# Performance work log

Measured on AMD Instinct MI355X. Metric: run time of the kernel, lower is better.

The kernel has to match this reference:

```python
import jax, jax.numpy as jnp
import numpy as np

B, M, D = 8, 8192, 1024   # batch, tokens, latent_dim
N, P = 128, 1             # num_experts, slots_per_expert
F = 4096                  # expert_dim


def setup_inputs() -> dict:
    key = jax.random.key(0)
    k_x, k_phi, k_w1, k_b1, k_w2, k_b2 = jax.random.split(key, 6)
    x = jax.random.normal(k_x, (B, M, D), dtype=jnp.float32)
    # phi initialized as randn(d, n, p) / sqrt(d) in the original
    phi = jax.random.normal(k_phi, (D, N, P), dtype=jnp.float32) / (D ** 0.5)
    # Single shared expert MLP (original aliases one nn.Sequential across all experts)
    W1 = jax.random.normal(k_w1, (D, F), dtype=jnp.float32) / (D ** 0.5)
    b1 = jax.random.normal(k_b1, (F,), dtype=jnp.float32) * 0.01
    W2 = jax.random.normal(k_w2, (F, D), dtype=jnp.float32) / (F ** 0.5)
    b2 = jax.random.normal(k_b2, (D,), dtype=jnp.float32) * 0.01
    return {"x": x, "phi": phi, "W1": W1, "b1": b1, "W2": W2, "b2": b2}


def reference(x, phi, W1, b1, W2, b2):
    # dispatch / combine logits: [b, m, n, p]
    logits = jnp.einsum('bmd,dnp->bmnp', x, phi)
    d = jax.nn.softmax(logits, axis=1)                      # softmax over tokens m
    b_, m_, n_, p_ = logits.shape
    c = jax.nn.softmax(logits.reshape(b_, m_, n_ * p_), axis=-1).reshape(b_, m_, n_, p_)
    # slot inputs: [b, n, p, d]
    x_i = jnp.einsum('bmd,bmnp->bnpd', x, d)
    # shared expert MLP (torch GELU default = exact erf)
    h = jax.nn.gelu(jnp.einsum('bnpd,df->bnpf', x_i, W1) + b1, approximate=False)
    y_i = jnp.einsum('bnpf,fd->bnpd', h, W2) + b2
    # combine: [b, m, d]
    y = jnp.einsum('bnpd,bmnp->bmd', y_i, c)
    return y
```

## Files before the change

### kernel.cpp

```cpp
#include <hip/hip_runtime.h>
#include <math.h>

#define Bq 8
#define Mq 8192
#define Dq 1024
#define Nq 128
#define Fq 4096

typedef __bf16 bf16x8 __attribute__((ext_vector_type(8)));
typedef float f32x4 __attribute__((ext_vector_type(4)));
union P4 { __bf16 h[4]; unsigned long long u; };
union H4 { short4 v; _Float16 h[4]; };
union B8 { int4 v; __bf16 h[8]; };

__device__ __forceinline__ int swz128(int row, int bcol) {
  return row * 128 + (bcol ^ ((row & 7) << 4));
}
__device__ __forceinline__ int swz256(int row, int bcol) {
  return row * 256 + (bcol ^ ((row & 7) << 4));
}
__device__ __forceinline__ int swzX(int row, int bcol) {
  return row * 128 + (bcol ^ ((((row & 7) ^ ((row >> 3) & 7))) << 4));
}

__global__ __launch_bounds__(256) void wconv(const float* __restrict__ src,
                                             unsigned long long* __restrict__ dst, long n4)
{
  long i = (long)blockIdx.x * 256 + threadIdx.x;
  if (i >= n4) return;
  float4 v = ((const float4*)src)[i];
  P4 p; p.h[0] = (__bf16)v.x; p.h[1] = (__bf16)v.y; p.h[2] = (__bf16)v.z; p.h[3] = (__bf16)v.w;
  dst[i] = p.u;
}

__global__ __launch_bounds__(256) void phi_conv(const float* __restrict__ src,
                                                __bf16* __restrict__ dst)
{
  int idx = blockIdx.x * 256 + threadIdx.x;
  int d = idx >> 7, n = idx & 127;
  dst[(long)n * Dq + d] = (__bf16)src[idx];
}

__global__ __launch_bounds__(256) void logits_mfma(
    const float* __restrict__ x, const __bf16* __restrict__ phiT,
    __bf16* __restrict__ eT, __bf16* __restrict__ cbuf)
{
  __shared__ __align__(16) char sA[16384];
  __shared__ __align__(16) char sP[16384];
  int mt = blockIdx.x, b = blockIdx.y;
  int m0 = mt * 128;
  int t = threadIdx.x;
  int arow = t >> 4, ac4 = t & 15;
  int prow = t >> 1, pc = (t & 1) * 4;
  int w = t >> 6, l = t & 63, la = l & 15, lb = l >> 4;

  f32x4 zero = {0.f, 0.f, 0.f, 0.f};
  f32x4 acc[2][8];
  for (int i = 0; i < 2; ++i) for (int j = 0; j < 8; ++j) acc[i][j] = zero;

  for (int k0 = 0; k0 < Dq; k0 += 64) {
    #pragma unroll
    for (int i = 0; i < 8; ++i) {
      int row = arow + 16 * i;
      float4 v = *(const float4*)(x + ((long)b * Mq + m0 + row) * Dq + k0 + ac4 * 4);
      P4 p;
      p.h[0] = (__bf16)v.x; p.h[1] = (__bf16)v.y;
      p.h[2] = (__bf16)v.z; p.h[3] = (__bf16)v.w;
      *(unsigned long long*)(sA + swz128(row, 8 * ac4)) = p.u;
    }
    {
      const __bf16* Pp = phiT + (long)prow * Dq + k0 + pc * 8;
      #pragma unroll
      for (int q = 0; q < 4; ++q)
        *(int4*)(sP + swz128(prow, (pc + q) * 16)) = *(const int4*)(Pp + q * 8);
    }
    __syncthreads();
    #pragma unroll
    for (int sub = 0; sub < 2; ++sub) {
      int mbyte = sub * 64 + lb * 16;
      bf16x8 af0 = *(const bf16x8*)(sA + swz128(w * 32 + la, mbyte));
      bf16x8 af1 = *(const bf16x8*)(sA + swz128(w * 32 + 16 + la, mbyte));
      bf16x8 bv[8];
      #pragma unroll
      for (int j = 0; j < 8; ++j)
        bv[j] = *(const bf16x8*)(sP + swz128(j * 16 + la, mbyte));
      #pragma unroll
      for (int j = 0; j < 8; ++j) {
        acc[0][j] = __builtin_amdgcn_mfma_f32_16x16x32_bf16(af0, bv[j], acc[0][j], 0, 0, 0);
        acc[1][j] = __builtin_amdgcn_mfma_f32_16x16x32_bf16(af1, bv[j], acc[1][j], 0, 0, 0);
      }
    }
    __syncthreads();
  }
  float inv[2][4];
  #pragma unroll
  for (int i = 0; i < 2; ++i)
    #pragma unroll
    for (int r = 0; r < 4; ++r) {
      float s = 0.f;
      #pragma unroll
      for (int j = 0; j < 8; ++j) s += __expf(acc[i][j][r]);
      s += __shfl_xor(s, 1); s += __shfl_xor(s, 2);
      s += __shfl_xor(s, 4); s += __shfl_xor(s, 8);
      inv[i][r] = 1.0f / s;
    }
  __bf16* Cb = cbuf + ((long)b * Mq + m0) * Nq;
  __bf16* Eb = eT + (long)b * Nq * Mq + m0;
  #pragma unroll
  for (int i = 0; i < 2; ++i)
    #pragma unroll
    for (int j = 0; j < 8; ++j) {
      P4 p;
      #pragma unroll
      for (int r = 0; r < 4; ++r) {
        int row = w * 32 + i * 16 + lb * 4 + r;
        float e = __expf(acc[i][j][r]);
        p.h[r] = (__bf16)e;
        Cb[(long)row * Nq + j * 16 + la] = (__bf16)(e * inv[i][r]);
      }
      *(unsigned long long*)(Eb + (long)(j * 16 + la) * Mq + w * 32 + i * 16 + lb * 4) = p.u;
    }
}

__global__ __launch_bounds__(256) void colsum_rows(const __bf16* __restrict__ eT,
                                                   float* __restrict__ cinv)
{
  __shared__ float red[4];
  int r = blockIdx.x;
  int t = threadIdx.x;
  const __bf16* p = eT + (long)r * Mq;
  float s = 0.f;
  #pragma unroll
  for (int k = 0; k < 4; ++k) {
    B8 v; v.v = *(const int4*)(p + t * 8 + k * 2048);
    #pragma unroll
    for (int e = 0; e < 8; ++e) s += (float)v.h[e];
  }
  #pragma unroll
  for (int off = 32; off >= 1; off >>= 1) s += __shfl_down(s, off);
  if ((t & 63) == 0) red[t >> 6] = s;
  __syncthreads();
  if (t == 0) cinv[r] = 1.0f / (red[0] + red[1] + red[2] + red[3]);
}

__global__ __launch_bounds__(256) void xi_mfma(
    const __bf16* __restrict__ eT, const float* __restrict__ x,
    _Float16* __restrict__ part)
{
  __shared__ __align__(16) char sD[16384];
  __shared__ __align__(16) char sX[16384];
  int lin = blockIdx.x;
  int wk = (lin & 7) * 64 + (lin >> 3);
  int dts = wk & 7, kc = (wk >> 3) & 7, b = wk >> 6;
  int d0 = dts * 128;
  int t = threadIdx.x;
  int w = t >> 6, l = t & 63, la = l & 15, lb = l >> 4;
  int arow = t >> 1, ahalf = t & 1;
  const __bf16* Ep0 = eT + ((long)b * Nq + arow) * Mq + kc * 1024 + ahalf * 32;
  int bmb = (w * 2 + (l >> 5)) * 8;
  int bd  = (l & 31) * 4;
  const float* Xp0 = x + ((long)b * Mq + kc * 1024 + bmb) * Dq + d0 + bd;

  f32x4 zero = {0.f, 0.f, 0.f, 0.f};
  f32x4 acc[2][8];
  for (int i = 0; i < 2; ++i) for (int j = 0; j < 8; ++j) acc[i][j] = zero;

  int4 ar[4];
  float br[8][4];
  #pragma unroll
  for (int q = 0; q < 4; ++q) ar[q] = *(const int4*)(Ep0 + q * 8);
  #pragma unroll
  for (int k = 0; k < 8; ++k) *(float4*)br[k] = *(const float4*)(Xp0 + (long)k * Dq);
  #pragma unroll
  for (int q = 0; q < 4; ++q) *(int4*)(sD + swzX(arow, ahalf * 64 + q * 16)) = ar[q];
  #pragma unroll
  for (int q = 0; q < 4; ++q) {
    B8 o;
    #pragma unroll
    for (int k = 0; k < 8; ++k) o.h[k] = (__bf16)br[k][q];
    *(int4*)(sX + swzX(bd + q, 2 * bmb)) = o.v;
  }

  for (int it = 0; it < 16; ++it) {
    __syncthreads();
    if (it < 15) {
      #pragma unroll
      for (int q = 0; q < 4; ++q) ar[q] = *(const int4*)(Ep0 + (it + 1) * 64 + q * 8);
      #pragma unroll
      for (int k = 0; k < 8; ++k)
        *(float4*)br[k] = *(const float4*)(Xp0 + ((long)(it + 1) * 64 + k) * Dq);
    }
    #pragma unroll
    for (int sub = 0; sub < 2; ++sub) {
      int mbyte = sub * 64 + lb * 16;
      bf16x8 af0 = *(const bf16x8*)(sD + swzX(w * 32 + la, mbyte));
      bf16x8 af1 = *(const bf16x8*)(sD + swzX(w * 32 + 16 + la, mbyte));
      #pragma unroll
      for (int j = 0; j < 8; ++j) {
        bf16x8 bv = *(const bf16x8*)(sX + swzX(j * 16 + la, mbyte));
        acc[0][j] = __builtin_amdgcn_mfma_f32_16x16x32_bf16(af0, bv, acc[0][j], 0, 0, 0);
        acc[1][j] = __builtin_amdgcn_mfma_f32_16x16x32_bf16(af1, bv, acc[1][j], 0, 0, 0);
      }
    }
    __syncthreads();
    if (it < 15) {
      #pragma unroll
      for (int q = 0; q < 4; ++q) *(int4*)(sD + swzX(arow, ahalf * 64 + q * 16)) = ar[q];
      #pragma unroll
      for (int q = 0; q < 4; ++q) {
        B8 o;
        #pragma unroll
        for (int k = 0; k < 8; ++k) o.h[k] = (__bf16)br[k][q];
        *(int4*)(sX + swzX(bd + q, 2 * bmb)) = o.v;
      }
    }
  }
  _Float16* P = part + (((long)kc * Bq + b) * 8 + dts) * 16384;
  #pragma unroll
  for (int i = 0; i < 2; ++i)
    #pragma unroll
    for (int j = 0; j < 8; ++j) {
      H4 o;
      #pragma unroll
      for (int r = 0; r < 4; ++r) o.h[r] = (_Float16)acc[i][j][r];
      *(short4*)(P + ((w * 16 + i * 8 + j) * 64 + l) * 4) = o.v;
    }
}

__global__ __launch_bounds__(256) void xi_reduce(const _Float16* __restrict__ part,
    const float* __restrict__ cinv, __bf16* __restrict__ xib)
{
  int s = blockIdx.x * 256 + threadIdx.x;
  int l = s & 63, j = (s >> 6) & 7, i = (s >> 9) & 1;
  int w = (s >> 10) & 3, dts = (s >> 12) & 7, b = s >> 15;
  const _Float16* p = part + ((long)b * 8 + dts) * 16384 + ((w * 16 + i * 8 + j) * 64 + l) * 4;
  float sum[4] = {};
  #pragma unroll
  for (int kc = 0; kc < 8; ++kc) {
    H4 v; v.v = *(const short4*)(p + (long)kc * 1048576);
    #pragma unroll
    for (int r = 0; r < 4; ++r) sum[r] += (float)v.h[r];
  }
  int lb = l >> 4, la = l & 15;
  int nbase = w * 32 + i * 16 + lb * 4;
  int d = dts * 128 + j * 16 + la;
  #pragma unroll
  for (int r = 0; r < 4; ++r) {
    int n = b * 128 + nbase + r;
    xib[(long)n * Dq + d] = (__bf16)(sum[r] * cinv[n]);
  }
}

template<int EPI, typename OT>
__global__ __launch_bounds__(256) void gemm_bf16(const __bf16* __restrict__ A,
    const __bf16* __restrict__ Bw, const float* __restrict__ bias,
    OT* __restrict__ C, int lda, int ldb, int ldc, int kLen, long strideCz)
{
  __shared__ __align__(16) char sA[16384];
  __shared__ __align__(16) char sB[16384];
  int m0 = blockIdx.x * 128, n0 = blockIdx.y * 128;
  int kbase = blockIdx.z * kLen;
  C += (long)blockIdx.z * strideCz;
  int t = threadIdx.x;
  int col = t & 127, half = t >> 7;
  int w = t >> 6, l = t & 63, la = l & 15, lb = l >> 4;

  f32x4 zero = {0.f, 0.f, 0.f, 0.f};
  f32x4 acc[2][8];
  for (int i = 0; i < 2; ++i) for (int j = 0; j < 8; ++j) acc[i][j] = zero;

  for (int kt = 0; kt < kLen; kt += 64) {
    int kp = kbase + kt;
    #pragma unroll
    for (int s = 0; s < 4; ++s) {
      int idx = t + 256 * s;
      int row = idx >> 3, c8 = idx & 7;
      *(int4*)(sA + swz128(row, c8 * 16)) =
          *(const int4*)(A + (long)(m0 + row) * lda + kp + c8 * 8);
    }
    {
      const __bf16* Bp = Bw + (long)(kp + half * 32) * ldb + n0 + col;
      #pragma unroll
      for (int i = 0; i < 32; i += 4) {
        P4 p;
        p.h[0] = Bp[(long)(i + 0) * ldb]; p.h[1] = Bp[(long)(i + 1) * ldb];
        p.h[2] = Bp[(long)(i + 2) * ldb]; p.h[3] = Bp[(long)(i + 3) * ldb];
        *(unsigned long long*)(sB + swz128(col, 2 * (half * 32 + i))) = p.u;
      }
    }
    __syncthreads();
    #pragma unroll
    for (int sub = 0; sub < 2; ++sub) {
      int mbyte = sub * 64 + lb * 16;
      bf16x8 af0 = *(const bf16x8*)(sA + swz128(w * 32 + la, mbyte));
      bf16x8 af1 = *(const bf16x8*)(sA + swz128(w * 32 + 16 + la, mbyte));
      bf16x8 bv[8];
      #pragma unroll
      for (int j = 0; j < 8; ++j)
        bv[j] = *(const bf16x8*)(sB + swz128(j * 16 + la, mbyte));
      #pragma unroll
      for (int j = 0; j < 8; ++j) {
        acc[0][j] = __builtin_amdgcn_mfma_f32_16x16x32_bf16(af0, bv[j], acc[0][j], 0, 0, 0);
        acc[1][j] = __builtin_amdgcn_mfma_f32_16x16x32_bf16(af1, bv[j], acc[1][j], 0, 0, 0);
      }
    }
    __syncthreads();
  }
  #pragma unroll
  for (int i = 0; i < 2; ++i)
    #pragma unroll
    for (int j = 0; j < 8; ++j)
      #pragma unroll
      for (int r = 0; r < 4; ++r) {
        int row = m0 + w * 32 + i * 16 + lb * 4 + r;
        int colg = n0 + j * 16 + la;
        float v = acc[i][j][r];
        if (EPI == 2) {
          v += bias[colg];
          v = 0.5f * v * (1.0f + erff(v * 0.70710678118654752f));
        }
        C[(long)row * ldc + colg] = (OT)v;
      }
}

__global__ __launch_bounds__(256) void g2_reduce(const float* __restrict__ part,
    const float* __restrict__ b2, __bf16* __restrict__ yiT)
{
  long idx = (long)blockIdx.x * 256 + threadIdx.x;
  int row = (int)(idx >> 10);
  int d = (int)(idx & 1023);
  float s = part[idx] + part[idx + 1048576] + part[idx + 2097152] + part[idx + 3145728] + b2[d];
  int b = row >> 7, n = row & 127;
  yiT[((long)b * Dq + d) * Nq + n] = (__bf16)s;
}

__global__ __launch_bounds__(256) void combine_mfma(const __bf16* __restrict__ cbuf,
    const __bf16* __restrict__ yiT, float* __restrict__ y)
{
  __shared__ __align__(16) char sC[32768];
  __shared__ __align__(16) char sY[32768];
  int lin = blockIdx.x;
  int wk = (lin & 7) * 512 + (lin >> 3);
  int dt = wk & 7, mt = (wk >> 3) & 63, b = wk >> 9;
  int m0 = mt * 128, d0 = dt * 128;
  int t = threadIdx.x;
  #pragma unroll
  for (int s = 0; s < 8; ++s) {
    int idx = t + 256 * s;
    int row = idx >> 4, c16 = idx & 15;
    *(int4*)(sC + swz256(row, c16 * 16)) =
        *(const int4*)(cbuf + ((long)b * Mq + m0 + row) * Nq + c16 * 8);
    *(int4*)(sY + swz256(row, c16 * 16)) =
        *(const int4*)(yiT + ((long)b * Dq + d0 + row) * Nq + c16 * 8);
  }
  __syncthreads();
  int w = t >> 6, l = t & 63, la = l & 15, lb = l >> 4;
  f32x4 zero = {0.f, 0.f, 0.f, 0.f};
  f32x4 acc[2][8];
  for (int i = 0; i < 2; ++i) for (int j = 0; j < 8; ++j) acc[i][j] = zero;
  #pragma unroll
  for (int sub = 0; sub < 4; ++sub) {
    int mbyte = sub * 64 + lb * 16;
    bf16x8 af0 = *(const bf16x8*)(sC + swz256(w * 32 + la, mbyte));
    bf16x8 af1 = *(const bf16x8*)(sC + swz256(w * 32 + 16 + la, mbyte));
    #pragma unroll
    for (int j = 0; j < 8; ++j) {
      bf16x8 bv = *(const bf16x8*)(sY + swz256(j * 16 + la, mbyte));
      acc[0][j] = __builtin_amdgcn_mfma_f32_16x16x32_bf16(af0, bv, acc[0][j], 0, 0, 0);
      acc[1][j] = __builtin_amdgcn_mfma_f32_16x16x32_bf16(af1, bv, acc[1][j], 0, 0, 0);
    }
  }
  float* Y = y + ((long)b * Mq + m0) * Dq + d0;
  #pragma unroll
  for (int i = 0; i < 2; ++i)
    #pragma unroll
    for (int j = 0; j < 8; ++j)
      #pragma unroll
      for (int r = 0; r < 4; ++r)
        Y[(long)(w * 32 + i * 16 + lb * 4 + r) * Dq + j * 16 + la] = acc[i][j][r];
}

extern "C" void kernel_launch(void* const* d_in, const int* in_sizes, int n_in,
                              void* d_out, int out_size, void* d_ws, size_t ws_size,
                              hipStream_t stream) {
  const float* x   = (const float*)d_in[0];
  const float* phi = (const float*)d_in[1];
  const float* W1  = (const float*)d_in[2];
  const float* b1  = (const float*)d_in[3];
  const float* W2  = (const float*)d_in[4];
  const float* b2  = (const float*)d_in[5];
  float* y = (float*)d_out;

  char* W = (char*)d_ws;
  __bf16*   cbuf   = (__bf16*)W;
  __bf16*   eT     = (__bf16*)(W + 16777216);
  __bf16*   h      = eT;
  _Float16* part   = (_Float16*)(W + 33554432);
  float*    g2part = (float*)(W + 33554432);
  __bf16*   W1b    = (__bf16*)(W + 50331648);
  __bf16*   W2b    = (__bf16*)(W + 58720256);
  __bf16*   xib    = (__bf16*)(W + 67108864);
  __bf16*   yiT    = (__bf16*)(W + 69206016);
  float*    cinv   = (float*)(W + 71303168);
  __bf16*   phiT   = (__bf16*)(W + 75497472);

  wconv<<<4096, 256, 0, stream>>>(W1, (unsigned long long*)W1b, 1048576);
  wconv<<<4096, 256, 0, stream>>>(W2, (unsigned long long*)W2b, 1048576);
  phi_conv<<<512, 256, 0, stream>>>(phi, phiT);
  logits_mfma<<<dim3(Mq / 128, Bq), 256, 0, stream>>>(x, phiT, eT, cbuf);
  colsum_rows<<<Bq * Nq, 256, 0, stream>>>(eT, cinv);
  xi_mfma<<<512, 256, 0, stream>>>(eT, x, part);
  xi_reduce<<<1024, 256, 0, stream>>>(part, cinv, xib);
  gemm_bf16<2, __bf16><<<dim3(8, 32, 1), 256, 0, stream>>>(
      xib, W1b, b1, h, Dq, Fq, Fq, 1024, 0L);
  gemm_bf16<0, float><<<dim3(8, 8, 4), 256, 0, stream>>>(
      h, W2b, nullptr, g2part, Fq, Dq, Dq, 1024, 1048576L);
  g2_reduce<<<4096, 256, 0, stream>>>(g2part, b2, yiT);
  combine_mfma<<<4096, 256, 0, stream>>>(cbuf, yiT, y);
}
```

Baseline: 365.1 us.

## Pre-transpose weights to bf16 and cache bf16 x copy for xi GEMM

```diff
diff --git a/kernel.cpp b/kernel.cpp
--- a/kernel.cpp
+++ b/kernel.cpp
@@ -12,6 +12,7 @@
 union P4 { __bf16 h[4]; unsigned long long u; };
 union H4 { short4 v; _Float16 h[4]; };
 union B8 { int4 v; __bf16 h[8]; };
+union U4 { ushort4 v; __bf16 h[4]; };
 
 __device__ __forceinline__ int swz128(int row, int bcol) {
   return row * 128 + (bcol ^ ((row & 7) << 4));
@@ -21,16 +22,6 @@
 }
 __device__ __forceinline__ int swzX(int row, int bcol) {
   return row * 128 + (bcol ^ ((((row & 7) ^ ((row >> 3) & 7))) << 4));
-}
-
-__global__ __launch_bounds__(256) void wconv(const float* __restrict__ src,
-                                             unsigned long long* __restrict__ dst, long n4)
-{
-  long i = (long)blockIdx.x * 256 + threadIdx.x;
-  if (i >= n4) return;
-  float4 v = ((const float4*)src)[i];
-  P4 p; p.h[0] = (__bf16)v.x; p.h[1] = (__bf16)v.y; p.h[2] = (__bf16)v.z; p.h[3] = (__bf16)v.w;
-  dst[i] = p.u;
 }
 
 __global__ __launch_bounds__(256) void phi_conv(const float* __restrict__ src,
@@ -41,9 +32,35 @@
   dst[(long)n * Dq + d] = (__bf16)src[idx];
 }
 
+__global__ __launch_bounds__(256) void wconvT(const float* __restrict__ src,
+                                              __bf16* __restrict__ dst, int R, int C)
+{
+  __shared__ __bf16 tile[64][66];
+  int c0 = blockIdx.x * 64, r0 = blockIdx.y * 64;
+  int t = threadIdx.x;
+  int row = t >> 2, cq = (t & 3) * 16;
+  const float* S = src + (long)(r0 + row) * C + c0 + cq;
+  #pragma unroll
+  for (int q = 0; q < 4; ++q) {
+    float4 v = *(const float4*)(S + q * 4);
+    tile[cq + q * 4 + 0][row] = (__bf16)v.x;
+    tile[cq + q * 4 + 1][row] = (__bf16)v.y;
+    tile[cq + q * 4 + 2][row] = (__bf16)v.z;
+    tile[cq + q * 4 + 3][row] = (__bf16)v.w;
+  }
+  __syncthreads();
+  __bf16* D = dst + (long)(c0 + row) * R + r0 + cq;
+  B8 o0, o1;
+  #pragma unroll
+  for (int e = 0; e < 8; ++e) { o0.h[e] = tile[row][cq + e]; o1.h[e] = tile[row][cq + 8 + e]; }
+  *(int4*)(D) = o0.v;
+  *(int4*)(D + 8) = o1.v;
+}
+
+template<bool WXB>
 __global__ __launch_bounds__(256) void logits_mfma(
     const float* __restrict__ x, const __bf16* __restrict__ phiT,
-    __bf16* __restrict__ eT, __bf16* __restrict__ cbuf)
+    __bf16* __restrict__ eT, __bf16* __restrict__ cbuf, __bf16* __restrict__ xb)
 {
   __shared__ __align__(16) char sA[16384];
   __shared__ __align__(16) char sP[16384];
@@ -67,6 +84,8 @@
       p.h[0] = (__bf16)v.x; p.h[1] = (__bf16)v.y;
       p.h[2] = (__bf16)v.z; p.h[3] = (__bf16)v.w;
       *(unsigned long long*)(sA + swz128(row, 8 * ac4)) = p.u;
+      if (WXB)
+        *(unsigned long long*)(xb + ((long)b * Mq + m0 + row) * Dq + k0 + ac4 * 4) = p.u;
     }
     {
       const __bf16* Pp = phiT + (long)prow * Dq + k0 + pc * 8;
@@ -143,8 +162,8 @@
   if (t == 0) cinv[r] = 1.0f / (red[0] + red[1] + red[2] + red[3]);
 }
 
-__global__ __launch_bounds__(256) void xi_mfma(
-    const __bf16* __restrict__ eT, const float* __restrict__ x,
+__global__ __launch_bounds__(256) void xi_mfma_xb(
+    const __bf16* __restrict__ eT, const __bf16* __restrict__ xb,
     _Float16* __restrict__ part)
 {
   __shared__ __align__(16) char sD[16384];
@@ -159,28 +178,111 @@
   const __bf16* Ep0 = eT + ((long)b * Nq + arow) * Mq + kc * 1024 + ahalf * 32;
   int bmb = (w * 2 + (l >> 5)) * 8;
   int bd  = (l & 31) * 4;
-  const float* Xp0 = x + ((long)b * Mq + kc * 1024 + bmb) * Dq + d0 + bd;
+  const __bf16* Xp0 = xb + ((long)b * Mq + kc * 1024 + bmb) * Dq + d0 + bd;
 
   f32x4 zero = {0.f, 0.f, 0.f, 0.f};
   f32x4 acc[2][8];
   for (int i = 0; i < 2; ++i) for (int j = 0; j < 8; ++j) acc[i][j] = zero;
 
   int4 ar[4];
-  float br[8][4];
+  U4 br[8];
   #pragma unroll
   for (int q = 0; q < 4; ++q) ar[q] = *(const int4*)(Ep0 + q * 8);
   #pragma unroll
-  for (int k = 0; k < 8; ++k) *(float4*)br[k] = *(const float4*)(Xp0 + (long)k * Dq);
+  for (int k = 0; k < 8; ++k) br[k].v = *(const ushort4*)(Xp0 + (long)k * Dq);
   #pragma unroll
   for (int q = 0; q < 4; ++q) *(int4*)(sD + swzX(arow, ahalf * 64 + q * 16)) = ar[q];
   #pragma unroll
   for (int q = 0; q < 4; ++q) {
     B8 o;
     #pragma unroll
+    for (int k = 0; k < 8; ++k) o.h[k] = br[k].h[q];
+    *(int4*)(sX + swzX(bd + q, 2 * bmb)) = o.v;
+  }
+
+  for (int it = 0; it < 16; ++it) {
+    __syncthreads();
+    if (it < 15) {
+      #pragma unroll
+      for (int q = 0; q < 4; ++q) ar[q] = *(const int4*)(Ep0 + (it + 1) * 64 + q * 8);
+      #pragma unroll
+      for (int k = 0; k < 8; ++k)
+        br[k].v = *(const ushort4*)(Xp0 + ((long)(it + 1) * 64 + k) * Dq);
+    }
+    #pragma unroll
+    for (int sub = 0; sub < 2; ++sub) {
+      int mbyte = sub * 64 + lb * 16;
+      bf16x8 af0 = *(const bf16x8*)(sD + swzX(w * 32 + la, mbyte));
+      bf16x8 af1 = *(const bf16x8*)(sD + swzX(w * 32 + 16 + la, mbyte));
+      #pragma unroll
+      for (int j = 0; j < 8; ++j) {
+        bf16x8 bv = *(const bf16x8*)(sX + swzX(j * 16 + la, mbyte));
+        acc[0][j] = __builtin_amdgcn_mfma_f32_16x16x32_bf16(af0, bv, acc[0][j], 0, 0, 0);
+        acc[1][j] = __builtin_amdgcn_mfma_f32_16x16x32_bf16(af1, bv, acc[1][j], 0, 0, 0);
+      }
+    }
+    __syncthreads();
+    if (it < 15) {
+      #pragma unroll
+      for (int q = 0; q < 4; ++q) *(int4*)(sD + swzX(arow, ahalf * 64 + q * 16)) = ar[q];
+      #pragma unroll
+      for (int q = 0; q < 4; ++q) {
+        B8 o;
+        #pragma unroll
+        for (int k = 0; k < 8; ++k) o.h[k] = br[k].h[q];
+        *(int4*)(sX + swzX(bd + q, 2 * bmb)) = o.v;
+      }
+    }
+  }
+  _Float16* P = part + (((long)kc * Bq + b) * 8 + dts) * 16384;
+  #pragma unroll
+  for (int i = 0; i < 2; ++i)
+    #pragma unroll
+    for (int j = 0; j < 8; ++j) {
+      H4 o;
+      #pragma unroll
+      for (int r = 0; r < 4; ++r) o.h[r] = (_Float16)acc[i][j][r];
+      *(short4*)(P + ((w * 16 + i * 8 + j) * 64 + l) * 4) = o.v;
+    }
+}
+
+__global__ __launch_bounds__(256) void xi_mfma_f32(
+    const __bf16* __restrict__ eT, const float* __restrict__ x,
+    _Float16* __restrict__ part)
+{
+  __shared__ __align__(16) char sD[16384];
+  __shared__ __align__(16) char sX[16384];
+  int lin = blockIdx.x;
+  int wk = (lin & 7) * 64 + (lin >> 3);
+  int dts = wk & 7, kc = (wk >> 3) & 7, b = wk >> 6;
+  int d0 = dts * 128;
+  int t = threadIdx.x;
+  int w = t >> 6, l = t & 63, la = l & 15, lb = l >> 4;
+  int arow = t >> 1, ahalf = t & 1;
+  const __bf16* Ep0 = eT + ((long)b * Nq + arow) * Mq + kc * 1024 + ahalf * 32;
+  int bmb = (w * 2 + (l >> 5)) * 8;
+  int bd  = (l & 31) * 4;
+  const float* Xp0 = x + ((long)b * Mq + kc * 1024 + bmb) * Dq + d0 + bd;
+
+  f32x4 zero = {0.f, 0.f, 0.f, 0.f};
+  f32x4 acc[2][8];
+  for (int i = 0; i < 2; ++i) for (int j = 0; j < 8; ++j) acc[i][j] = zero;
+
+  int4 ar[4];
+  float br[8][4];
+  #pragma unroll
+  for (int q = 0; q < 4; ++q) ar[q] = *(const int4*)(Ep0 + q * 8);
+  #pragma unroll
+  for (int k = 0; k < 8; ++k) *(float4*)br[k] = *(const float4*)(Xp0 + (long)k * Dq);
+  #pragma unroll
+  for (int q = 0; q < 4; ++q) *(int4*)(sD + swzX(arow, ahalf * 64 + q * 16)) = ar[q];
+  #pragma unroll
+  for (int q = 0; q < 4; ++q) {
+    B8 o;
+    #pragma unroll
     for (int k = 0; k < 8; ++k) o.h[k] = (__bf16)br[k][q];
     *(int4*)(sX + swzX(bd + q, 2 * bmb)) = o.v;
   }
-
   for (int it = 0; it < 16; ++it) {
     __syncthreads();
     if (it < 15) {
@@ -252,8 +354,8 @@
 }
 
 template<int EPI, typename OT>
-__global__ __launch_bounds__(256) void gemm_bf16(const __bf16* __restrict__ A,
-    const __bf16* __restrict__ Bw, const float* __restrict__ bias,
+__global__ __launch_bounds__(256) void gemm_tt(const __bf16* __restrict__ A,
+    const __bf16* __restrict__ BT, const float* __restrict__ bias,
     OT* __restrict__ C, int lda, int ldb, int ldc, int kLen, long strideCz)
 {
   __shared__ __align__(16) char sA[16384];
@@ -262,7 +364,6 @@
   int kbase = blockIdx.z * kLen;
   C += (long)blockIdx.z * strideCz;
   int t = threadIdx.x;
-  int col = t & 127, half = t >> 7;
   int w = t >> 6, l = t & 63, la = l & 15, lb = l >> 4;
 
   f32x4 zero = {0.f, 0.f, 0.f, 0.f};
@@ -277,16 +378,8 @@
       int row = idx >> 3, c8 = idx & 7;
       *(int4*)(sA + swz128(row, c8 * 16)) =
           *(const int4*)(A + (long)(m0 + row) * lda + kp + c8 * 8);
-    }
-    {
-      const __bf16* Bp = Bw + (long)(kp + half * 32) * ldb + n0 + col;
-      #pragma unroll
-      for (int i = 0; i < 32; i += 4) {
-        P4 p;
-        p.h[0] = Bp[(long)(i + 0) * ldb]; p.h[1] = Bp[(long)(i + 1) * ldb];
-        p.h[2] = Bp[(long)(i + 2) * ldb]; p.h[3] = Bp[(long)(i + 3) * ldb];
-        *(unsigned long long*)(sB + swz128(col, 2 * (half * 32 + i))) = p.u;
-      }
+      *(int4*)(sB + swz128(row, c8 * 16)) =
+          *(const int4*)(BT + (long)(n0 + row) * ldb + kp + c8 * 8);
     }
     __syncthreads();
     #pragma unroll
@@ -397,24 +490,30 @@
   __bf16*   h      = eT;
   _Float16* part   = (_Float16*)(W + 33554432);
   float*    g2part = (float*)(W + 33554432);
-  __bf16*   W1b    = (__bf16*)(W + 50331648);
-  __bf16*   W2b    = (__bf16*)(W + 58720256);
+  __bf16*   W1T    = (__bf16*)(W + 50331648);
+  __bf16*   W2T    = (__bf16*)(W + 58720256);
   __bf16*   xib    = (__bf16*)(W + 67108864);
   __bf16*   yiT    = (__bf16*)(W + 69206016);
   float*    cinv   = (float*)(W + 71303168);
-  __bf16*   phiT   = (__bf16*)(W + 75497472);
-
-  wconv<<<4096, 256, 0, stream>>>(W1, (unsigned long long*)W1b, 1048576);
-  wconv<<<4096, 256, 0, stream>>>(W2, (unsigned long long*)W2b, 1048576);
+  __bf16*   phiT   = (__bf16*)(W + 72351744);
+  __bf16*   xb     = (__bf16*)(W + 73400320);
+  bool big = ws_size >= 207618048ull;
+
+  wconvT<<<dim3(Fq / 64, Dq / 64), 256, 0, stream>>>(W1, W1T, Dq, Fq);
+  wconvT<<<dim3(Dq / 64, Fq / 64), 256, 0, stream>>>(W2, W2T, Fq, Dq);
   phi_conv<<<512, 256, 0, stream>>>(phi, phiT);
-  logits_mfma<<<dim3(Mq / 128, Bq), 256, 0, stream>>>(x, phiT, eT, cbuf);
+  if (big)
+    logits_mfma<true><<<dim3(Mq / 128, Bq), 256, 0, stream>>>(x, phiT, eT, cbuf, xb);
+  else
+    logits_mfma<false><<<dim3(Mq / 128, Bq), 256, 0, stream>>>(x, phiT, eT, cbuf, nullptr);
   colsum_rows<<<Bq * Nq, 256, 0, stream>>>(eT, cinv);
-  xi_mfma<<<512, 256, 0, stream>>>(eT, x, part);
+  if (big) xi_mfma_xb<<<512, 256, 0, stream>>>(eT, xb, part);
+  else     xi_mfma_f32<<<512, 256, 0, stream>>>(eT, x, part);
   xi_reduce<<<1024, 256, 0, stream>>>(part, cinv, xib);
-  gemm_bf16<2, __bf16><<<dim3(8, 32, 1), 256, 0, stream>>>(
-      xib, W1b, b1, h, Dq, Fq, Fq, 1024, 0L);
-  gemm_bf16<0, float><<<dim3(8, 8, 4), 256, 0, stream>>>(
-      h, W2b, nullptr, g2part, Fq, Dq, Dq, 1024, 1048576L);
+  gemm_tt<2, __bf16><<<dim3(8, 32, 1), 256, 0, stream>>>(
+      xib, W1T, b1, h, Dq, Dq, Fq, 1024, 0L);
+  gemm_tt<0, float><<<dim3(8, 8, 4), 256, 0, stream>>>(
+      h, W2T, nullptr, g2part, Fq, Fq, Dq, 1024, 1048576L);
   g2_reduce<<<4096, 256, 0, stream>>>(g2part, b2, yiT);
   combine_mfma<<<4096, 256, 0, stream>>>(cbuf, yiT, y);
 }
```

New measurement: 366.0 us. Within noise of the previous version (+0.2%).
